# Kernel tuning notes

Measured on AMD Instinct MI355X. Metric: run time of the kernel, lower is better.

The kernel has to match this reference:

```python
import jax, jax.numpy as jnp
import numpy as np

TWO_PI = 2.0 * np.pi
SIGMA = 25.0  # marginal_prob_std sigma


def marginal_prob_std(t):
    # std(t) = sqrt((sigma^{2t} - 1) / (2 ln sigma)) for VE-SDE
    return jnp.sqrt((SIGMA ** (2.0 * t) - 1.0) / (2.0 * np.log(SIGMA)))


def edge_conv(x, src, dst, W1, b1, W2, b2, num_nodes):
    # PyG EdgeConv: msg = mlp(cat([x_i, x_j - x_i])), x_i = x[dst], x_j = x[src];
    # scatter-max over dst. First linear split so concat is never materialized:
    # cat([x_i, x_j - x_i]) @ W1 = x_i @ (Wa - Wb) + x_j @ Wb
    d = x.shape[-1]
    Wa, Wb = W1[:d], W1[d:]
    h_center = x @ (Wa - Wb)        # [N, H]
    h_nbr = x @ Wb                  # [N, H]
    e = jax.nn.relu(h_center[dst] + h_nbr[src] + b1)  # [E, H]
    e = e @ W2 + b2                 # [E, out]
    return jax.ops.segment_max(e, dst, num_segments=num_nodes)


def setup_inputs() -> dict:
    N, E, B, H, EM = 50000, 500000, 1024, 128, 64
    CLS, SD, GD, WD = 10, 4, 2, 2
    key = jax.random.key(0)
    ks = jax.random.split(key, 32)

    def lin(k, fi, fo):
        return jax.random.normal(k, (fi, fo), jnp.float32) / np.sqrt(fi)

    inp = {
        "t": jax.random.uniform(ks[0], (N, 1), jnp.float32, 1e-3, 1.0),
        "obj_x": jax.random.normal(ks[1], (N, SD), jnp.float32),
        "obj_geo": jax.random.normal(ks[2], (N, GD), jnp.float32),
        "wall": jax.random.normal(ks[3], (B, WD), jnp.float32),
        "category": jax.random.randint(ks[4], (N,), 0, CLS),
        "batch_idx": jnp.sort(jax.random.randint(ks[5], (N,), 0, B)),
        "src": jax.random.randint(ks[6], (E,), 0, N),
        "dst": jnp.tile(jnp.arange(N), E // N),  # every node receives edges
        "embed_W": jax.random.normal(ks[7], (CLS, EM), jnp.float32),
        "gfp_W": jax.random.normal(ks[8], (EM // 2,), jnp.float32) * 30.0,
        "sW": lin(ks[9], EM, EM), "sb": jnp.zeros((EM,), jnp.float32),
        "w1": lin(ks[10], WD, EM), "wb1": jnp.zeros((EM,), jnp.float32),
        "w2": lin(ks[11], EM, EM), "wb2": jnp.zeros((EM,), jnp.float32),
        "i1": lin(ks[12], SD + GD, H), "ib1": jnp.zeros((H,), jnp.float32),
        "i2": lin(ks[13], H, H), "ib2": jnp.zeros((H,), jnp.float32),
        "m1W1": lin(ks[14], 2 * (H + 3 * EM), H), "m1b1": jnp.zeros((H,), jnp.float32),
        "m1W2": lin(ks[15], H, H), "m1b2": jnp.zeros((H,), jnp.float32),
        "m2W1": lin(ks[16], 2 * (H + 3 * EM), H), "m2b1": jnp.zeros((H,), jnp.float32),
        "m2W2": lin(ks[17], H, SD), "m2b2": jnp.zeros((SD,), jnp.float32),
    }
    return inp


def reference(t, obj_x, obj_geo, wall, category, batch_idx, src, dst,
              embed_W, gfp_W, sW, sb, w1, wb1, w2, wb2,
              i1, ib1, i2, ib2, m1W1, m1b1, m1W2, m1b2,
              m2W1, m2b1, m2W2, m2b2):
    N = obj_x.shape[0]
    # conditioning features
    class_feat = jax.nn.relu(embed_W[category])                       # [N, EM]
    tv = t[:, 0]                                                      # [N]
    x_proj = tv[:, None] * gfp_W[None, :] * TWO_PI                    # [N, EM/2]
    gfp = jnp.concatenate([jnp.sin(x_proj), jnp.cos(x_proj)], axis=-1)
    sigma_feat = jax.nn.relu(gfp @ sW + sb)                           # [N, EM]
    wall_h = jax.nn.relu(jax.nn.relu(wall @ w1 + wb1) @ w2 + wb2)     # [B, EM]
    wall_feat = wall_h[batch_idx]                                     # [N, EM]
    cond = jnp.concatenate([class_feat, sigma_feat, wall_feat], axis=-1)

    # init encoder
    xin = jnp.concatenate([obj_x, obj_geo], axis=-1)                  # [N, 6]
    init = jax.nn.relu(jax.nn.relu(xin @ i1 + ib1) @ i2 + ib2)        # [N, H]

    # main backbone: two EdgeConvs with conditioning concat
    x = jnp.concatenate([init, cond], axis=-1)                        # [N, H+3EM]
    x = jax.nn.relu(edge_conv(x, src, dst, m1W1, m1b1, m1W2, m1b2, N))
    x = jnp.concatenate([x, cond], axis=-1)                           # [N, H+3EM]
    x = edge_conv(x, src, dst, m2W1, m2b1, m2W2, m2b2, N)             # [N, 4]

    return x / (marginal_prob_std(t) + 1e-7)
```

## Files before the change

### kernel.cpp

```cpp
#include <hip/hip_runtime.h>
#include <math.h>

#define NTHREADS 256
#define TWO_PI_F 6.28318530717958647692f
#define LOG_SIGMA 3.2188758248682006f

typedef unsigned short u16;
typedef unsigned int u32;
typedef _Float16 f16x2 __attribute__((ext_vector_type(2)));
typedef _Float16 f16x8 __attribute__((ext_vector_type(8)));
typedef float f32x4 __attribute__((ext_vector_type(4)));

#define MFMA16(a, b, c) __builtin_amdgcn_mfma_f32_16x16x32_f16((a), (b), (c), 0, 0, 0)

__device__ __forceinline__ u16 f2h(float f) {
  _Float16 h = (_Float16)f;
  union { _Float16 h; u16 u; } cv;
  cv.h = h;
  return cv.u;
}
__device__ __forceinline__ f16x2 relu2(f16x2 x) {
  f16x2 z;
  z[0] = (_Float16)0.f; z[1] = (_Float16)0.f;
  return __builtin_elementwise_max(x, z);
}

__global__ __launch_bounds__(256) void prep_kernel(
    const float* __restrict__ m1W2, const float* __restrict__ m1W1,
    const float* __restrict__ m2W1, const float* __restrict__ sW,
    const float* __restrict__ i1, const float* __restrict__ i2,
    const float* __restrict__ m2W2,
    u16* __restrict__ m1W2t, u16* __restrict__ Wc1t, u16* __restrict__ Wc2t,
    u16* __restrict__ sWt, u16* __restrict__ i1t, u16* __restrict__ i2t,
    u16* __restrict__ m2W2t) {
  int idx = blockIdx.x * 256 + threadIdx.x;
  if (idx < 16384) {
    int n = idx >> 7, k = idx & 127;
    m1W2t[idx] = f2h(m1W2[k * 128 + n]);
  } else if (idx < 98304) {
    int j = idx - 16384;
    int n = j / 320, k = j - n * 320;
    float v = (n < 128) ? (m1W1[k * 128 + n] - m1W1[(320 + k) * 128 + n])
                        : m1W1[(320 + k) * 128 + (n - 128)];
    Wc1t[j] = f2h(v);
  } else if (idx < 180224) {
    int j = idx - 98304;
    int n = j / 320, k = j - n * 320;
    float v = (n < 128) ? (m2W1[k * 128 + n] - m2W1[(320 + k) * 128 + n])
                        : m2W1[(320 + k) * 128 + (n - 128)];
    Wc2t[j] = f2h(v);
  } else if (idx < 184320) {
    int j = idx - 180224;
    int n = j >> 6, k = j & 63;
    sWt[j] = f2h(sW[k * 64 + n]);
  } else if (idx < 188416) {
    int j = idx - 184320;
    int n = j >> 5, k = j & 31;
    i1t[j] = (k < 6) ? f2h(i1[k * 128 + n]) : (u16)0;
  } else if (idx < 204800) {
    int j = idx - 188416;
    int n = j >> 7, k = j & 127;
    i2t[j] = f2h(i2[k * 128 + n]);
  } else if (idx < 205312) {
    int j = idx - 204800;
    int n = j >> 7, k = j & 127;
    m2W2t[j] = f2h(m2W2[k * 4 + n]);
  }
}

__global__ void wall_kernel(const float* __restrict__ wall,
                            const float* __restrict__ w1, const float* __restrict__ wb1,
                            const float* __restrict__ w2, const float* __restrict__ wb2,
                            float* __restrict__ wall_h) {
  __shared__ float h1[64];
  int b = blockIdx.x;
  int f = threadIdx.x;
  float v = wall[b * 2 + 0] * w1[f] + wall[b * 2 + 1] * w1[64 + f] + wb1[f];
  h1[f] = fmaxf(v, 0.f);
  __syncthreads();
  float acc = wb2[f];
  for (int k = 0; k < 64; ++k) acc = fmaf(h1[k], w2[k * 64 + f], acc);
  wall_h[b * 64 + f] = fmaxf(acc, 0.f);
}

__global__ __launch_bounds__(256) void node_kernel(
    const float* __restrict__ t, const float* __restrict__ obj_x,
    const float* __restrict__ obj_geo,
    const int* __restrict__ category, const int* __restrict__ batch_idx,
    const float* __restrict__ embed_W, const float* __restrict__ gfp_W,
    const u16* __restrict__ sWt, const float* __restrict__ sb,
    const u16* __restrict__ i1t, const float* __restrict__ ib1,
    const u16* __restrict__ i2t, const float* __restrict__ ib2,
    const u16* __restrict__ Wc1t, const float* __restrict__ m1b1,
    const float* __restrict__ wall_h,
    u16* __restrict__ hc1f, u16* __restrict__ hn1f,
    u16* __restrict__ cond_h, int N) {
  __shared__ u16 xb[64 * 328];
  __shared__ u16 ab[64 * 136];
  __shared__ float t_s[64];
  __shared__ int cat_s[64];
  __shared__ int bid_s[64];

  const int tid = threadIdx.x;
  const int base = blockIdx.x * 64;
  const int wave = tid >> 6, lane = tid & 63;
  const int ln16 = lane & 15, q8 = lane >> 4;

  f16x8 bs0 = *(const f16x8*)(sWt + (size_t)((wave * 16 + ln16) * 64) + q8 * 8);
  f16x8 bs1 = *(const f16x8*)(sWt + (size_t)((wave * 16 + ln16) * 64) + 32 + q8 * 8);
  f16x8 bh[2];
#pragma unroll
  for (int nt = 0; nt < 2; ++nt)
    bh[nt] = *(const f16x8*)(i1t + (size_t)((wave * 32 + nt * 16 + ln16) * 32) + q8 * 8);

  if (tid < 64) {
    int node = min(base + tid, N - 1);
    t_s[tid] = t[node];
    cat_s[tid] = category[node];
    bid_s[tid] = batch_idx[node];
  }
  __syncthreads();

  for (int idx = tid; idx < 64 * 32; idx += NTHREADS) {
    int row = idx >> 5, k = idx & 31;
    float xp = t_s[row] * gfp_W[k] * TWO_PI_F;
    float s, c;
    sincosf(xp, &s, &c);
    ab[row * 136 + k] = f2h(s);
    ab[row * 136 + 32 + k] = f2h(c);
  }
  for (int idx = tid; idx < 64 * 64; idx += NTHREADS) {
    int row = idx >> 6, f = idx & 63;
    xb[row * 328 + 128 + f] = f2h(fmaxf(embed_W[cat_s[row] * 64 + f], 0.f));
    xb[row * 328 + 256 + f] = f2h(wall_h[bid_s[row] * 64 + f]);
  }
  __syncthreads();

  f32x4 cs[4];
#pragma unroll
  for (int mt = 0; mt < 4; ++mt) cs[mt] = (f32x4)0.f;
#pragma unroll
  for (int mt = 0; mt < 4; ++mt) {
    f16x8 a0 = *(const f16x8*)&ab[(mt * 16 + ln16) * 136 + q8 * 8];
    cs[mt] = MFMA16(a0, bs0, cs[mt]);
  }
#pragma unroll
  for (int mt = 0; mt < 4; ++mt) {
    f16x8 a1 = *(const f16x8*)&ab[(mt * 16 + ln16) * 136 + 32 + q8 * 8];
    cs[mt] = MFMA16(a1, bs1, cs[mt]);
  }
  __syncthreads();

  {
    int col = wave * 16 + ln16;
    float bias = sb[col];
#pragma unroll
    for (int mt = 0; mt < 4; ++mt)
#pragma unroll
      for (int r = 0; r < 4; ++r)
        xb[(mt * 16 + q8 * 4 + r) * 328 + 192 + col] = f2h(fmaxf(cs[mt][r] + bias, 0.f));
  }
  for (int idx = tid; idx < 64 * 32; idx += NTHREADS) {
    int row = idx >> 5, k = idx & 31;
    int node = min(base + row, N - 1);
    float v = (k < 4) ? obj_x[node * 4 + k] : ((k < 6) ? obj_geo[node * 2 + (k - 4)] : 0.f);
    ab[row * 136 + k] = f2h(v);
  }
  __syncthreads();

  for (int idx = tid; idx < 64 * 24; idx += NTHREADS) {
    int row = idx / 24, q = idx - row * 24;
    int node = base + row;
    if (node < N)
      *(uint4*)&cond_h[(size_t)node * 192 + q * 8] = *(uint4*)&xb[row * 328 + 128 + q * 8];
  }

  f32x4 ch[2][4];
#pragma unroll
  for (int nt = 0; nt < 2; ++nt)
#pragma unroll
    for (int mt = 0; mt < 4; ++mt) ch[nt][mt] = (f32x4)0.f;
#pragma unroll
  for (int mt = 0; mt < 4; ++mt) {
    f16x8 a = *(const f16x8*)&ab[(mt * 16 + ln16) * 136 + q8 * 8];
#pragma unroll
    for (int nt = 0; nt < 2; ++nt) ch[nt][mt] = MFMA16(a, bh[nt], ch[nt][mt]);
  }
  f16x8 bcur2[2], bnext2[2];
#pragma unroll
  for (int nt = 0; nt < 2; ++nt)
    bcur2[nt] = *(const f16x8*)(i2t + (size_t)((wave * 32 + nt * 16 + ln16) * 128) + q8 * 8);
  __syncthreads();
#pragma unroll
  for (int nt = 0; nt < 2; ++nt) {
    int col = wave * 32 + nt * 16 + ln16;
    float bias = ib1[col];
#pragma unroll
    for (int mt = 0; mt < 4; ++mt)
#pragma unroll
      for (int r = 0; r < 4; ++r)
        ab[(mt * 16 + q8 * 4 + r) * 136 + col] = f2h(fmaxf(ch[nt][mt][r] + bias, 0.f));
  }
  __syncthreads();

  f32x4 ci[2][4];
#pragma unroll
  for (int nt = 0; nt < 2; ++nt)
#pragma unroll
    for (int mt = 0; mt < 4; ++mt) ci[nt][mt] = (f32x4)0.f;
  for (int kt = 0; kt < 4; ++kt) {
    if (kt < 3) {
#pragma unroll
      for (int nt = 0; nt < 2; ++nt)
        bnext2[nt] = *(const f16x8*)(i2t + (size_t)((wave * 32 + nt * 16 + ln16) * 128) +
                                     (kt + 1) * 32 + q8 * 8);
    }
#pragma unroll
    for (int mt = 0; mt < 4; ++mt) {
      f16x8 a = *(const f16x8*)&ab[(mt * 16 + ln16) * 136 + kt * 32 + q8 * 8];
#pragma unroll
      for (int nt = 0; nt < 2; ++nt) ci[nt][mt] = MFMA16(a, bcur2[nt], ci[nt][mt]);
    }
#pragma unroll
    for (int nt = 0; nt < 2; ++nt) bcur2[nt] = bnext2[nt];
  }
#pragma unroll
  for (int nt = 0; nt < 2; ++nt) {
    int col = wave * 32 + nt * 16 + ln16;
    float bias = ib2[col];
#pragma unroll
    for (int mt = 0; mt < 4; ++mt)
#pragma unroll
      for (int r = 0; r < 4; ++r)
        xb[(mt * 16 + q8 * 4 + r) * 328 + col] = f2h(fmaxf(ci[nt][mt][r] + bias, 0.f));
  }
  __syncthreads();

  f32x4 c2[4][4];
#pragma unroll
  for (int nt = 0; nt < 4; ++nt)
#pragma unroll
    for (int mt = 0; mt < 4; ++mt) c2[nt][mt] = (f32x4)0.f;
  f16x8 bcur[4], bnext[4];
#pragma unroll
  for (int nt = 0; nt < 4; ++nt)
    bcur[nt] = *(const f16x8*)(Wc1t + (size_t)((wave * 64 + nt * 16 + ln16) * 320) + q8 * 8);
  for (int kt = 0; kt < 10; ++kt) {
    if (kt < 9) {
#pragma unroll
      for (int nt = 0; nt < 4; ++nt)
        bnext[nt] = *(const f16x8*)(Wc1t + (size_t)((wave * 64 + nt * 16 + ln16) * 320) +
                                    (kt + 1) * 32 + q8 * 8);
    }
#pragma unroll
    for (int mt = 0; mt < 4; ++mt) {
      f16x8 a = *(const f16x8*)&xb[(mt * 16 + ln16) * 328 + kt * 32 + q8 * 8];
#pragma unroll
      for (int nt = 0; nt < 4; ++nt) c2[nt][mt] = MFMA16(a, bcur[nt], c2[nt][mt]);
    }
#pragma unroll
    for (int nt = 0; nt < 4; ++nt) bcur[nt] = bnext[nt];
  }
#pragma unroll
  for (int nt = 0; nt < 4; ++nt) {
    int col = wave * 64 + nt * 16 + ln16;
#pragma unroll
    for (int mt = 0; mt < 4; ++mt)
#pragma unroll
      for (int r = 0; r < 4; ++r) {
        int node = base + mt * 16 + q8 * 4 + r;
        if (node < N) {
          if (col < 128)
            hc1f[(size_t)node * 128 + col] = f2h(c2[nt][mt][r] + m1b1[col]);
          else
            hn1f[(size_t)node * 128 + (col - 128)] = f2h(c2[nt][mt][r]);
        }
      }
  }
}

__global__ __launch_bounds__(256, 3) void edge1_kernel(
    const u16* __restrict__ hc1f, const u16* __restrict__ hn1f,
    const u16* __restrict__ cond_h, const int* __restrict__ src,
    const u16* __restrict__ m1W2t, const float* __restrict__ m1b2,
    const u16* __restrict__ Wc2t, const float* __restrict__ m2b1,
    u16* __restrict__ hc2f, u16* __restrict__ hn2f, int N) {
  __shared__ u16 x2_lds[32 * 328];
  __shared__ int sid[320];

  const int tid = threadIdx.x;
  const int base = blockIdx.x * 32;
  const int wave = tid >> 6, lane = tid & 63;
  const int ln16 = lane & 15, q8 = lane >> 4;
  const int rowoff = (wave >> 1) * 16;
  const int colh = (wave & 1) * 64;
  const int myrow = rowoff + ln16;
  const int mynode = min(base + myrow, N - 1);

  for (int idx = tid; idx < 320; idx += NTHREADS) {
    int e = idx >> 5, n = idx & 31;
    sid[idx] = src[min(base + n, N - 1) + e * N];
  }
  for (int idx = tid; idx < 768; idx += NTHREADS) {
    int n = idx / 24, q = idx - n * 24;
    int nd = min(base + n, N - 1);
    *(uint4*)&x2_lds[n * 328 + 128 + q * 8] = *(const uint4*)&cond_h[(size_t)nd * 192 + q * 8];
  }

  uint4 hc4[4];
#pragma unroll
  for (int kt = 0; kt < 4; ++kt)
    hc4[kt] = *(const uint4*)&hc1f[(size_t)mynode * 128 + kt * 32 + q8 * 8];

  f16x8 bfr[4][4];
#pragma unroll
  for (int nt = 0; nt < 4; ++nt)
#pragma unroll
    for (int kt = 0; kt < 4; ++kt)
      bfr[nt][kt] = *(const f16x8*)(m1W2t + (size_t)(colh + nt * 16 + ln16) * 128 +
                                    kt * 32 + q8 * 8);
  __syncthreads();

  f32x4 ymax[4];
#pragma unroll
  for (int nt = 0; nt < 4; ++nt)
#pragma unroll
    for (int r = 0; r < 4; ++r) ymax[nt][r] = -3.0e38f;

  uint4 g[4], gn[4];
  {
    int s = sid[myrow];
#pragma unroll
    for (int kt = 0; kt < 4; ++kt)
      g[kt] = *(const uint4*)&hn1f[(size_t)s * 128 + kt * 32 + q8 * 8];
  }
  for (int e = 0; e < 10; ++e) {
    if (e < 9) {
      int s = sid[(e + 1) * 32 + myrow];
#pragma unroll
      for (int kt = 0; kt < 4; ++kt)
        gn[kt] = *(const uint4*)&hn1f[(size_t)s * 128 + kt * 32 + q8 * 8];
    }
#pragma unroll
    for (int kt = 0; kt < 4; ++kt) {
      f16x2* gp = (f16x2*)&g[kt];
      const f16x2* hp = (const f16x2*)&hc4[kt];
#pragma unroll
      for (int p = 0; p < 4; ++p) gp[p] = relu2(gp[p] + hp[p]);
    }
    f32x4 c[4];
#pragma unroll
    for (int nt = 0; nt < 4; ++nt) c[nt] = (f32x4)0.f;
#pragma unroll
    for (int kt = 0; kt < 4; ++kt) {
      f16x8 a = *(const f16x8*)&g[kt];
#pragma unroll
      for (int nt = 0; nt < 4; ++nt) c[nt] = MFMA16(a, bfr[nt][kt], c[nt]);
    }
#pragma unroll
    for (int nt = 0; nt < 4; ++nt)
#pragma unroll
      for (int r = 0; r < 4; ++r) ymax[nt][r] = fmaxf(ymax[nt][r], c[nt][r]);
#pragma unroll
    for (int kt = 0; kt < 4; ++kt) g[kt] = gn[kt];
  }

#pragma unroll
  for (int nt = 0; nt < 4; ++nt) {
    int col = colh + nt * 16 + ln16;
    float bias = m1b2[col];
#pragma unroll
    for (int r = 0; r < 4; ++r) {
      int row = rowoff + q8 * 4 + r;
      x2_lds[row * 328 + col] = f2h(fmaxf(ymax[nt][r] + bias, 0.f));
    }
  }
  __syncthreads();

  f32x4 c2[2][4];
#pragma unroll
  for (int mt = 0; mt < 2; ++mt)
#pragma unroll
    for (int nt = 0; nt < 4; ++nt) c2[mt][nt] = (f32x4)0.f;
  f16x8 bcur[4], bnext[4];
#pragma unroll
  for (int nt = 0; nt < 4; ++nt)
    bcur[nt] = *(const f16x8*)(Wc2t + (size_t)(wave * 64 + nt * 16 + ln16) * 320 + q8 * 8);
  for (int kt = 0; kt < 10; ++kt) {
    if (kt < 9) {
#pragma unroll
      for (int nt = 0; nt < 4; ++nt)
        bnext[nt] = *(const f16x8*)(Wc2t + (size_t)(wave * 64 + nt * 16 + ln16) * 320 +
                                    (kt + 1) * 32 + q8 * 8);
    }
    f16x8 a0 = *(const f16x8*)&x2_lds[ln16 * 328 + kt * 32 + q8 * 8];
    f16x8 a1 = *(const f16x8*)&x2_lds[(16 + ln16) * 328 + kt * 32 + q8 * 8];
#pragma unroll
    for (int nt = 0; nt < 4; ++nt) {
      c2[0][nt] = MFMA16(a0, bcur[nt], c2[0][nt]);
      c2[1][nt] = MFMA16(a1, bcur[nt], c2[1][nt]);
    }
#pragma unroll
    for (int nt = 0; nt < 4; ++nt) bcur[nt] = bnext[nt];
  }
#pragma unroll
  for (int nt = 0; nt < 4; ++nt) {
    int col = wave * 64 + nt * 16 + ln16;
#pragma unroll
    for (int mt = 0; mt < 2; ++mt)
#pragma unroll
      for (int r = 0; r < 4; ++r) {
        int node = base + mt * 16 + q8 * 4 + r;
        if (node < N) {
          if (col < 128)
            hc2f[(size_t)node * 128 + col] = f2h(c2[mt][nt][r] + m2b1[col]);
          else
            hn2f[(size_t)node * 128 + (col - 128)] = f2h(c2[mt][nt][r]);
        }
      }
  }
}

__global__ __launch_bounds__(256) void edge2_kernel(
    const u16* __restrict__ hc2f, const u16* __restrict__ hn2f,
    const int* __restrict__ src, const float* __restrict__ t,
    const u16* __restrict__ m2W2t, const float* __restrict__ m2b2,
    float* __restrict__ out, int N) {
  const int tid = threadIdx.x;
  const int base = blockIdx.x * 32;
  const int ln = tid >> 3, kq = tid & 7;
  const int node = min(base + ln, N - 1);

  uint4 hc0 = *(const uint4*)&hc2f[(size_t)node * 128 + kq * 16];
  uint4 hc1_ = *(const uint4*)&hc2f[(size_t)node * 128 + kq * 16 + 8];
  uint4 w4[4][2];
#pragma unroll
  for (int j = 0; j < 4; ++j) {
    w4[j][0] = *(const uint4*)&m2W2t[j * 128 + kq * 16];
    w4[j][1] = *(const uint4*)&m2W2t[j * 128 + kq * 16 + 8];
  }
  float ymax[4] = {-3.0e38f, -3.0e38f, -3.0e38f, -3.0e38f};

  int s = src[node];
  uint4 g0 = *(const uint4*)&hn2f[(size_t)s * 128 + kq * 16];
  uint4 g1 = *(const uint4*)&hn2f[(size_t)s * 128 + kq * 16 + 8];
  for (int e = 0; e < 10; ++e) {
    f16x2 a2[8];
    {
      const f16x2* gp0 = (const f16x2*)&g0;
      const f16x2* gp1 = (const f16x2*)&g1;
      const f16x2* hp0 = (const f16x2*)&hc0;
      const f16x2* hp1 = (const f16x2*)&hc1_;
#pragma unroll
      for (int p = 0; p < 4; ++p) a2[p] = relu2(gp0[p] + hp0[p]);
#pragma unroll
      for (int p = 0; p < 4; ++p) a2[4 + p] = relu2(gp1[p] + hp1[p]);
    }
    if (e < 9) {
      s = src[node + (e + 1) * N];
      g0 = *(const uint4*)&hn2f[(size_t)s * 128 + kq * 16];
      g1 = *(const uint4*)&hn2f[(size_t)s * 128 + kq * 16 + 8];
    }
    float acc[4] = {0.f, 0.f, 0.f, 0.f};
#pragma unroll
    for (int j = 0; j < 4; ++j) {
      const f16x2* wp0 = (const f16x2*)&w4[j][0];
      const f16x2* wp1 = (const f16x2*)&w4[j][1];
#pragma unroll
      for (int p = 0; p < 4; ++p) {
        acc[j] = __builtin_amdgcn_fdot2(a2[p], wp0[p], acc[j], false);
        acc[j] = __builtin_amdgcn_fdot2(a2[4 + p], wp1[p], acc[j], false);
      }
    }
#pragma unroll
    for (int mask = 1; mask <= 4; mask <<= 1)
#pragma unroll
      for (int j = 0; j < 4; ++j) acc[j] += __shfl_xor(acc[j], mask);
#pragma unroll
    for (int j = 0; j < 4; ++j) ymax[j] = fmaxf(ymax[j], acc[j]);
  }
  if (kq < 4 && base + ln < N) {
    float tv = t[node];
    float mps = sqrtf((expf(2.f * tv * LOG_SIGMA) - 1.f) * (1.f / (2.f * LOG_SIGMA)));
    out[(size_t)node * 4 + kq] = (ymax[kq] + m2b2[kq]) / (mps + 1e-7f);
  }
}

extern "C" void kernel_launch(void* const* d_in, const int* in_sizes, int n_in,
                              void* d_out, int out_size, void* d_ws, size_t ws_size,
                              hipStream_t stream) {
  const float* t = (const float*)d_in[0];
  const float* obj_x = (const float*)d_in[1];
  const float* obj_geo = (const float*)d_in[2];
  const float* wall = (const float*)d_in[3];
  const int* category = (const int*)d_in[4];
  const int* batch_idx = (const int*)d_in[5];
  const int* src = (const int*)d_in[6];
  const float* embed_W = (const float*)d_in[8];
  const float* gfp_W = (const float*)d_in[9];
  const float* sW = (const float*)d_in[10];
  const float* sb = (const float*)d_in[11];
  const float* w1 = (const float*)d_in[12];
  const float* wb1 = (const float*)d_in[13];
  const float* w2 = (const float*)d_in[14];
  const float* wb2 = (const float*)d_in[15];
  const float* i1 = (const float*)d_in[16];
  const float* ib1 = (const float*)d_in[17];
  const float* i2 = (const float*)d_in[18];
  const float* ib2 = (const float*)d_in[19];
  const float* m1W1 = (const float*)d_in[20];
  const float* m1b1 = (const float*)d_in[21];
  const float* m1W2 = (const float*)d_in[22];
  const float* m1b2 = (const float*)d_in[23];
  const float* m2W1 = (const float*)d_in[24];
  const float* m2b1 = (const float*)d_in[25];
  const float* m2W2 = (const float*)d_in[26];
  const float* m2b2 = (const float*)d_in[27];
  float* out = (float*)d_out;

  const int N = in_sizes[0];
  const int B = in_sizes[3] / 2;

  char* w = (char*)d_ws;
  float* wall_h = (float*)w; w += (size_t)B * 64 * 4;
  u16* cond_h = (u16*)w;    w += (size_t)N * 192 * 2;
  u16* hc1f = (u16*)w;      w += (size_t)N * 128 * 2;
  u16* hn1f = (u16*)w;      w += (size_t)N * 128 * 2;
  u16* hc2f = (u16*)w;      w += (size_t)N * 128 * 2;
  u16* hn2f = (u16*)w;      w += (size_t)N * 128 * 2;
  u16* m1W2t = (u16*)w;     w += (size_t)128 * 128 * 2;
  u16* Wc1t = (u16*)w;      w += (size_t)256 * 320 * 2;
  u16* Wc2t = (u16*)w;      w += (size_t)256 * 320 * 2;
  u16* sWt = (u16*)w;       w += (size_t)64 * 64 * 2;
  u16* i1t = (u16*)w;       w += (size_t)128 * 32 * 2;
  u16* i2t = (u16*)w;       w += (size_t)128 * 128 * 2;
  u16* m2W2t = (u16*)w;     w += (size_t)4 * 128 * 2;

  prep_kernel<<<dim3(802), dim3(256), 0, stream>>>(m1W2, m1W1, m2W1, sW, i1, i2, m2W2,
                                                   m1W2t, Wc1t, Wc2t, sWt, i1t, i2t, m2W2t);
  wall_kernel<<<dim3(B), dim3(64), 0, stream>>>(wall, w1, wb1, w2, wb2, wall_h);
  node_kernel<<<dim3((N + 63) / 64), dim3(NTHREADS), 0, stream>>>(
      t, obj_x, obj_geo, category, batch_idx, embed_W, gfp_W, sWt, sb,
      i1t, ib1, i2t, ib2, Wc1t, m1b1, wall_h, hc1f, hn1f, cond_h, N);
  edge1_kernel<<<dim3((N + 31) / 32), dim3(NTHREADS), 0, stream>>>(
      hc1f, hn1f, cond_h, src, m1W2t, m1b2, Wc2t, m2b1, hc2f, hn2f, N);
  edge2_kernel<<<dim3((N + 31) / 32), dim3(NTHREADS), 0, stream>>>(
      hc2f, hn2f, src, t, m2W2t, m2b2, out, N);
}
```

Baseline: 301.9 us.

## Split edge1 into gather-max and separate conv2 GEMM; deepen gather prefetch to two edges

```diff
diff --git a/kernel.cpp b/kernel.cpp
--- a/kernel.cpp
+++ b/kernel.cpp
@@ -279,15 +279,11 @@
   }
 }
 
-__global__ __launch_bounds__(256, 3) void edge1_kernel(
+__global__ __launch_bounds__(256) void edge1_kernel(
     const u16* __restrict__ hc1f, const u16* __restrict__ hn1f,
-    const u16* __restrict__ cond_h, const int* __restrict__ src,
-    const u16* __restrict__ m1W2t, const float* __restrict__ m1b2,
-    const u16* __restrict__ Wc2t, const float* __restrict__ m2b1,
-    u16* __restrict__ hc2f, u16* __restrict__ hn2f, int N) {
-  __shared__ u16 x2_lds[32 * 328];
+    const int* __restrict__ src, const u16* __restrict__ m1W2t,
+    const float* __restrict__ m1b2, u16* __restrict__ y, int N) {
   __shared__ int sid[320];
-
   const int tid = threadIdx.x;
   const int base = blockIdx.x * 32;
   const int wave = tid >> 6, lane = tid & 63;
@@ -301,11 +297,6 @@
     int e = idx >> 5, n = idx & 31;
     sid[idx] = src[min(base + n, N - 1) + e * N];
   }
-  for (int idx = tid; idx < 768; idx += NTHREADS) {
-    int n = idx / 24, q = idx - n * 24;
-    int nd = min(base + n, N - 1);
-    *(uint4*)&x2_lds[n * 328 + 128 + q * 8] = *(const uint4*)&cond_h[(size_t)nd * 192 + q * 8];
-  }
 
   uint4 hc4[4];
 #pragma unroll
@@ -327,33 +318,40 @@
 #pragma unroll
     for (int r = 0; r < 4; ++r) ymax[nt][r] = -3.0e38f;
 
-  uint4 g[4], gn[4];
+  uint4 g[2][4];
   {
-    int s = sid[myrow];
-#pragma unroll
-    for (int kt = 0; kt < 4; ++kt)
-      g[kt] = *(const uint4*)&hn1f[(size_t)s * 128 + kt * 32 + q8 * 8];
-  }
+    int s0 = sid[myrow];
+    int s1 = sid[32 + myrow];
+#pragma unroll
+    for (int kt = 0; kt < 4; ++kt) {
+      g[0][kt] = *(const uint4*)&hn1f[(size_t)s0 * 128 + kt * 32 + q8 * 8];
+      g[1][kt] = *(const uint4*)&hn1f[(size_t)s1 * 128 + kt * 32 + q8 * 8];
+    }
+  }
+#pragma unroll
   for (int e = 0; e < 10; ++e) {
-    if (e < 9) {
-      int s = sid[(e + 1) * 32 + myrow];
+    const int sl = e & 1;
+    uint4 a4[4];
+#pragma unroll
+    for (int kt = 0; kt < 4; ++kt) {
+      f16x2* ap = (f16x2*)&a4[kt];
+      const f16x2* gp = (const f16x2*)&g[sl][kt];
+      const f16x2* hp = (const f16x2*)&hc4[kt];
+#pragma unroll
+      for (int p = 0; p < 4; ++p) ap[p] = relu2(gp[p] + hp[p]);
+    }
+    if (e + 2 < 10) {
+      int s = sid[(e + 2) * 32 + myrow];
 #pragma unroll
       for (int kt = 0; kt < 4; ++kt)
-        gn[kt] = *(const uint4*)&hn1f[(size_t)s * 128 + kt * 32 + q8 * 8];
-    }
+        g[sl][kt] = *(const uint4*)&hn1f[(size_t)s * 128 + kt * 32 + q8 * 8];
+    }
+    f32x4 c[4];
+#pragma unroll
+    for (int nt = 0; nt < 4; ++nt) c[nt] = (f32x4)0.f;
 #pragma unroll
     for (int kt = 0; kt < 4; ++kt) {
-      f16x2* gp = (f16x2*)&g[kt];
-      const f16x2* hp = (const f16x2*)&hc4[kt];
-#pragma unroll
-      for (int p = 0; p < 4; ++p) gp[p] = relu2(gp[p] + hp[p]);
-    }
-    f32x4 c[4];
-#pragma unroll
-    for (int nt = 0; nt < 4; ++nt) c[nt] = (f32x4)0.f;
-#pragma unroll
-    for (int kt = 0; kt < 4; ++kt) {
-      f16x8 a = *(const f16x8*)&g[kt];
+      f16x8 a = *(const f16x8*)&a4[kt];
 #pragma unroll
       for (int nt = 0; nt < 4; ++nt) c[nt] = MFMA16(a, bfr[nt][kt], c[nt]);
     }
@@ -361,8 +359,6 @@
     for (int nt = 0; nt < 4; ++nt)
 #pragma unroll
       for (int r = 0; r < 4; ++r) ymax[nt][r] = fmaxf(ymax[nt][r], c[nt][r]);
-#pragma unroll
-    for (int kt = 0; kt < 4; ++kt) g[kt] = gn[kt];
   }
 
 #pragma unroll
@@ -371,34 +367,55 @@
     float bias = m1b2[col];
 #pragma unroll
     for (int r = 0; r < 4; ++r) {
-      int row = rowoff + q8 * 4 + r;
-      x2_lds[row * 328 + col] = f2h(fmaxf(ymax[nt][r] + bias, 0.f));
-    }
-  }
-  __syncthreads();
-
-  f32x4 c2[2][4];
-#pragma unroll
-  for (int mt = 0; mt < 2; ++mt)
-#pragma unroll
-    for (int nt = 0; nt < 4; ++nt) c2[mt][nt] = (f32x4)0.f;
+      int node = base + rowoff + q8 * 4 + r;
+      if (node < N) y[(size_t)node * 128 + col] = f2h(fmaxf(ymax[nt][r] + bias, 0.f));
+    }
+  }
+}
+
+__global__ __launch_bounds__(256) void conv2_kernel(
+    const u16* __restrict__ y, const u16* __restrict__ cond_h,
+    const u16* __restrict__ Wc2t, const float* __restrict__ m2b1,
+    u16* __restrict__ hc2f, u16* __restrict__ hn2f, int N) {
+  __shared__ u16 xb[64 * 328];
+  const int tid = threadIdx.x;
+  const int base = blockIdx.x * 64;
+  const int wave = tid >> 6, lane = tid & 63;
+  const int ln16 = lane & 15, q8 = lane >> 4;
+
+  for (int idx = tid; idx < 64 * 16; idx += NTHREADS) {
+    int row = idx >> 4, q = idx & 15;
+    int nd = min(base + row, N - 1);
+    *(uint4*)&xb[row * 328 + q * 8] = *(const uint4*)&y[(size_t)nd * 128 + q * 8];
+  }
+  for (int idx = tid; idx < 64 * 24; idx += NTHREADS) {
+    int row = idx / 24, q = idx - row * 24;
+    int nd = min(base + row, N - 1);
+    *(uint4*)&xb[row * 328 + 128 + q * 8] = *(const uint4*)&cond_h[(size_t)nd * 192 + q * 8];
+  }
+  __syncthreads();
+
+  f32x4 c2[4][4];
+#pragma unroll
+  for (int nt = 0; nt < 4; ++nt)
+#pragma unroll
+    for (int mt = 0; mt < 4; ++mt) c2[nt][mt] = (f32x4)0.f;
   f16x8 bcur[4], bnext[4];
 #pragma unroll
   for (int nt = 0; nt < 4; ++nt)
-    bcur[nt] = *(const f16x8*)(Wc2t + (size_t)(wave * 64 + nt * 16 + ln16) * 320 + q8 * 8);
+    bcur[nt] = *(const f16x8*)(Wc2t + (size_t)((wave * 64 + nt * 16 + ln16) * 320) + q8 * 8);
   for (int kt = 0; kt < 10; ++kt) {
     if (kt < 9) {
 #pragma unroll
       for (int nt = 0; nt < 4; ++nt)
-        bnext[nt] = *(const f16x8*)(Wc2t + (size_t)(wave * 64 + nt * 16 + ln16) * 320 +
+        bnext[nt] = *(const f16x8*)(Wc2t + (size_t)((wave * 64 + nt * 16 + ln16) * 320) +
                                     (kt + 1) * 32 + q8 * 8);
     }
-    f16x8 a0 = *(const f16x8*)&x2_lds[ln16 * 328 + kt * 32 + q8 * 8];
-    f16x8 a1 = *(const f16x8*)&x2_lds[(16 + ln16) * 328 + kt * 32 + q8 * 8];
-#pragma unroll
-    for (int nt = 0; nt < 4; ++nt) {
-      c2[0][nt] = MFMA16(a0, bcur[nt], c2[0][nt]);
-      c2[1][nt] = MFMA16(a1, bcur[nt], c2[1][nt]);
+#pragma unroll
+    for (int mt = 0; mt < 4; ++mt) {
+      f16x8 a = *(const f16x8*)&xb[(mt * 16 + ln16) * 328 + kt * 32 + q8 * 8];
+#pragma unroll
+      for (int nt = 0; nt < 4; ++nt) c2[nt][mt] = MFMA16(a, bcur[nt], c2[nt][mt]);
     }
 #pragma unroll
     for (int nt = 0; nt < 4; ++nt) bcur[nt] = bnext[nt];
@@ -407,15 +424,15 @@
   for (int nt = 0; nt < 4; ++nt) {
     int col = wave * 64 + nt * 16 + ln16;
 #pragma unroll
-    for (int mt = 0; mt < 2; ++mt)
+    for (int mt = 0; mt < 4; ++mt)
 #pragma unroll
       for (int r = 0; r < 4; ++r) {
         int node = base + mt * 16 + q8 * 4 + r;
         if (node < N) {
           if (col < 128)
-            hc2f[(size_t)node * 128 + col] = f2h(c2[mt][nt][r] + m2b1[col]);
+            hc2f[(size_t)node * 128 + col] = f2h(c2[nt][mt][r] + m2b1[col]);
           else
-            hn2f[(size_t)node * 128 + (col - 128)] = f2h(c2[mt][nt][r]);
+            hn2f[(size_t)node * 128 + (col - 128)] = f2h(c2[nt][mt][r]);
         }
       }
   }
@@ -441,14 +458,22 @@
   }
   float ymax[4] = {-3.0e38f, -3.0e38f, -3.0e38f, -3.0e38f};
 
-  int s = src[node];
-  uint4 g0 = *(const uint4*)&hn2f[(size_t)s * 128 + kq * 16];
-  uint4 g1 = *(const uint4*)&hn2f[(size_t)s * 128 + kq * 16 + 8];
+  uint4 g[2][2];
+  {
+    int s0 = src[node];
+    int s1 = src[node + N];
+    g[0][0] = *(const uint4*)&hn2f[(size_t)s0 * 128 + kq * 16];
+    g[0][1] = *(const uint4*)&hn2f[(size_t)s0 * 128 + kq * 16 + 8];
+    g[1][0] = *(const uint4*)&hn2f[(size_t)s1 * 128 + kq * 16];
+    g[1][1] = *(const uint4*)&hn2f[(size_t)s1 * 128 + kq * 16 + 8];
+  }
+#pragma unroll
   for (int e = 0; e < 10; ++e) {
+    const int sl = e & 1;
     f16x2 a2[8];
     {
-      const f16x2* gp0 = (const f16x2*)&g0;
-      const f16x2* gp1 = (const f16x2*)&g1;
+      const f16x2* gp0 = (const f16x2*)&g[sl][0];
+      const f16x2* gp1 = (const f16x2*)&g[sl][1];
       const f16x2* hp0 = (const f16x2*)&hc0;
       const f16x2* hp1 = (const f16x2*)&hc1_;
 #pragma unroll
@@ -456,10 +481,10 @@
 #pragma unroll
       for (int p = 0; p < 4; ++p) a2[4 + p] = relu2(gp1[p] + hp1[p]);
     }
-    if (e < 9) {
-      s = src[node + (e + 1) * N];
-      g0 = *(const uint4*)&hn2f[(size_t)s * 128 + kq * 16];
-      g1 = *(const uint4*)&hn2f[(size_t)s * 128 + kq * 16 + 8];
+    if (e + 2 < 10) {
+      int s = src[node + (e + 2) * N];
+      g[sl][0] = *(const uint4*)&hn2f[(size_t)s * 128 + kq * 16];
+      g[sl][1] = *(const uint4*)&hn2f[(size_t)s * 128 + kq * 16 + 8];
     }
     float acc[4] = {0.f, 0.f, 0.f, 0.f};
 #pragma unroll
@@ -528,6 +553,7 @@
   u16* hn1f = (u16*)w;      w += (size_t)N * 128 * 2;
   u16* hc2f = (u16*)w;      w += (size_t)N * 128 * 2;
   u16* hn2f = (u16*)w;      w += (size_t)N * 128 * 2;
+  u16* yb = (u16*)w;        w += (size_t)N * 128 * 2;
   u16* m1W2t = (u16*)w;     w += (size_t)128 * 128 * 2;
   u16* Wc1t = (u16*)w;      w += (size_t)256 * 320 * 2;
   u16* Wc2t = (u16*)w;      w += (size_t)256 * 320 * 2;
@@ -543,7 +569,9 @@
       t, obj_x, obj_geo, category, batch_idx, embed_W, gfp_W, sWt, sb,
       i1t, ib1, i2t, ib2, Wc1t, m1b1, wall_h, hc1f, hn1f, cond_h, N);
   edge1_kernel<<<dim3((N + 31) / 32), dim3(NTHREADS), 0, stream>>>(
-      hc1f, hn1f, cond_h, src, m1W2t, m1b2, Wc2t, m2b1, hc2f, hn2f, N);
+      hc1f, hn1f, src, m1W2t, m1b2, yb, N);
+  conv2_kernel<<<dim3((N + 63) / 64), dim3(NTHREADS), 0, stream>>>(
+      yb, cond_h, Wc2t, m2b1, hc2f, hn2f, N);
   edge2_kernel<<<dim3((N + 31) / 32), dim3(NTHREADS), 0, stream>>>(
       hc2f, hn2f, src, t, m2W2t, m2b2, out, N);
 }
```

After: 332.6 us. +10.2%, slower.
